# Kernel tuning notes

Hardware: AMD Instinct MI355X
Metric: run time of the kernel (lower is better)

## Reference

```python
import jax, jax.numpy as jnp
import numpy as np

B, IN_DIM, H, E, V, MAX_LEN = 512, 1024, 512, 512, 2048, 32


def setup_inputs() -> dict:
    key = jax.random.key(0)
    ks = jax.random.split(key, 12)
    s = lambda k, shape, scale: (jax.random.normal(k, shape, dtype=jnp.float32) * scale)
    return {
        'x': jax.random.normal(ks[0], (B, IN_DIM), dtype=jnp.float32),
        'agent_w': s(ks[1], (IN_DIM, H), 1.0 / np.sqrt(IN_DIM)),
        'agent_b': jnp.zeros((H,), jnp.float32),
        'sos_embedding': s(ks[2], (E,), 0.01),  # reset_parameters: normal(0, 0.01)
        'embedding': s(ks[3], (V, E), 1.0),
        'w_ih': s(ks[4], (E, 4 * H), 1.0 / np.sqrt(H)),
        'w_hh': s(ks[5], (H, 4 * H), 1.0 / np.sqrt(H)),
        'b_ih': jnp.zeros((4 * H,), jnp.float32),
        'b_hh': jnp.zeros((4 * H,), jnp.float32),
        'out_w': s(ks[6], (H, V), 1.0 / np.sqrt(H)),
        'out_b': jnp.zeros((V,), jnp.float32),
    }


def _unroll(x, agent_w, agent_b, sos_embedding, embedding, w_ih, w_hh, b_ih, b_hh, out_w, out_b):
    h0 = x @ agent_w + agent_b              # agent provides initial hidden [B, H]
    c0 = jnp.zeros_like(h0)
    e0 = jnp.broadcast_to(sos_embedding, (x.shape[0], sos_embedding.shape[0]))
    key0 = jax.random.key(1)

    def step(carry, _):
        h, c, e, key = carry
        key, sk = jax.random.split(key)
        gates = e @ w_ih + h @ w_hh + (b_ih + b_hh)          # [B, 4H], torch gate order i,f,g,o
        i_g, f_g, g_g, o_g = jnp.split(gates, 4, axis=-1)
        c = jax.nn.sigmoid(f_g) * c + jax.nn.sigmoid(i_g) * jnp.tanh(g_g)
        h = jax.nn.sigmoid(o_g) * jnp.tanh(c)
        step_logits = jax.nn.log_softmax(h @ out_w + out_b, axis=-1)  # [B, V]
        probs = jnp.exp(step_logits)
        entropy = -jnp.sum(probs * step_logits, axis=-1)              # Categorical entropy
        sym = jax.random.categorical(sk, step_logits, axis=-1)        # sample [B]
        log_prob = jnp.take_along_axis(step_logits, sym[:, None], axis=1)[:, 0]
        e = embedding[sym]
        return (h, c, e, key), (sym, log_prob, entropy, probs)

    _, (seq, logp, ent, probs) = jax.lax.scan(step, (h0, c0, e0, key0), None, length=MAX_LEN)
    # scan emits leading time dim -> [B, L, ...]
    seq = jnp.transpose(seq, (1, 0))
    logp = jnp.transpose(logp, (1, 0))
    ent = jnp.transpose(ent, (1, 0))
    probs = jnp.transpose(probs, (1, 0, 2))
    # append EOS step (zeros; probs row of ones, as in the source)
    zcol = jnp.zeros((seq.shape[0], 1), jnp.float32)
    seq = jnp.concatenate([seq, zcol.astype(seq.dtype)], axis=1)
    logp = jnp.concatenate([logp, zcol], axis=1)
    ent = jnp.concatenate([ent, zcol], axis=1)
    probs = jnp.concatenate([probs, jnp.ones((probs.shape[0], 1, probs.shape[2]), probs.dtype)], axis=1)
    return seq, probs, logp, ent


def reference(x, agent_w, agent_b, sos_embedding, embedding, w_ih, w_hh, b_ih, b_hh, out_w, out_b):
    return _unroll(x, agent_w, agent_b, sos_embedding, embedding, w_ih, w_hh, b_ih, b_hh, out_w, out_b)
```

## Files before the change

### kernel.cpp

```cpp
#include <hip/hip_runtime.h>
#include <math.h>
#include <stdint.h>
#include <stddef.h>

#define B_ 512
#define H_ 512
#define E_ 512
#define V_ 2048
#define IN_ 1024
#define LSTEPS 32
#define LP1 33

#define TF_PARTITIONABLE 1

#define SPLITK 4
#define SPLITK_H0 16
#define PSTRIDE_GATES (B_ * 2048)
#define PSTRIDE_H0 (B_ * H_)

typedef unsigned short u16;
typedef __attribute__((ext_vector_type(8))) short bhalf8;
typedef __attribute__((ext_vector_type(4))) float f32x4;

__device__ __forceinline__ void tf2x32(uint32_t k0, uint32_t k1,
                                       uint32_t x0, uint32_t x1,
                                       uint32_t& o0, uint32_t& o1) {
  uint32_t ks2 = k0 ^ k1 ^ 0x1BD11BDAu;
  x0 += k0; x1 += k1;
#define TFR(R) { x0 += x1; x1 = (x1 << (R)) | (x1 >> (32 - (R))); x1 ^= x0; }
  TFR(13) TFR(15) TFR(26) TFR(6)
  x0 += k1; x1 += ks2 + 1u;
  TFR(17) TFR(29) TFR(16) TFR(24)
  x0 += ks2; x1 += k0 + 2u;
  TFR(13) TFR(15) TFR(26) TFR(6)
  x0 += k0; x1 += k1 + 3u;
  TFR(17) TFR(29) TFR(16) TFR(24)
  x0 += k1; x1 += ks2 + 4u;
  TFR(13) TFR(15) TFR(26) TFR(6)
  x0 += ks2; x1 += k0 + 5u;
#undef TFR
  o0 = x0; o1 = x1;
}

__global__ void init_keys_kernel(uint32_t* __restrict__ sk) {
  uint32_t k0 = 0u, k1 = 1u;
  for (int t = 0; t < LSTEPS; t++) {
    uint32_t a0, a1, b0, b1;
#if TF_PARTITIONABLE
    tf2x32(k0, k1, 0u, 0u, a0, a1);
    tf2x32(k0, k1, 0u, 1u, b0, b1);
    sk[2 * t] = b0; sk[2 * t + 1] = b1;
    k0 = a0; k1 = a1;
#else
    tf2x32(k0, k1, 0u, 2u, a0, a1);
    tf2x32(k0, k1, 1u, 3u, b0, b1);
    sk[2 * t] = a1; sk[2 * t + 1] = b1;
    k0 = a0; k1 = b0;
#endif
  }
}

__device__ __forceinline__ void split3(float v, u16& h, u16& m, u16& l) {
  uint32_t u = __float_as_uint(v);
  uint32_t r = (u + 0x7FFFu + ((u >> 16) & 1u)) >> 16;
  h = (u16)r;
  float res = v - __uint_as_float(r << 16);
  uint32_t u2 = __float_as_uint(res);
  uint32_t r2 = (u2 + 0x7FFFu + ((u2 >> 16) & 1u)) >> 16;
  m = (u16)r2;
  float res2 = res - __uint_as_float(r2 << 16);
  uint32_t u3 = __float_as_uint(res2);
  uint32_t r3 = (u3 + 0x7FFFu + ((u3 >> 16) & 1u)) >> 16;
  l = (u16)r3;
}

__global__ __launch_bounds__(256) void init_state_planes_kernel(
    const float* __restrict__ sos, float* __restrict__ c,
    u16* __restrict__ eh, u16* __restrict__ em, u16* __restrict__ el) {
  int idx = blockIdx.x * 256 + threadIdx.x;
  if (idx < B_ * H_) {
    c[idx] = 0.0f;
    u16 a, b2, d;
    split3(sos[idx & (E_ - 1)], a, b2, d);
    eh[idx] = a; em[idx] = b2; el[idx] = d;
  }
}

__global__ __launch_bounds__(256) void eos_fill_kernel(
    float* __restrict__ o_seq, float* __restrict__ o_probs,
    float* __restrict__ o_logp, float* __restrict__ o_ent) {
  int b = blockIdx.x, tid = threadIdx.x;
  float* pr = o_probs + ((size_t)b * LP1 + LSTEPS) * V_;
  for (int v = tid; v < V_; v += 256) pr[v] = 1.0f;
  if (tid == 0) {
    o_seq[b * LP1 + LSTEPS] = 0.0f;
    o_logp[b * LP1 + LSTEPS] = 0.0f;
    o_ent[b * LP1 + LSTEPS] = 0.0f;
  }
}

__global__ __launch_bounds__(256) void split_kernel(
    const float* __restrict__ src,
    u16* __restrict__ dh, u16* __restrict__ dm, u16* __restrict__ dl, int n) {
  int i = blockIdx.x * 256 + threadIdx.x;
  if (i < n) {
    u16 a, b2, d;
    split3(src[i], a, b2, d);
    dh[i] = a; dm[i] = b2; dl[i] = d;
  }
}

__global__ __launch_bounds__(256) void transpose_split_kernel(
    const float* __restrict__ src, int srcN,
    u16* __restrict__ dh, u16* __restrict__ dm, u16* __restrict__ dl,
    int dstK, int kOff) {
  __shared__ float t[32][33];
  int tx = threadIdx.x & 31, ty = threadIdx.x >> 5;
  int kt = blockIdx.x * 32, nt = blockIdx.y * 32;
#pragma unroll
  for (int j = 0; j < 4; j++)
    t[ty + j * 8][tx] = src[(size_t)(kt + ty + j * 8) * srcN + nt + tx];
  __syncthreads();
#pragma unroll
  for (int j = 0; j < 4; j++) {
    int n = nt + ty + j * 8;
    int k = kt + tx;
    u16 a, b2, d;
    split3(t[tx][ty + j * 8], a, b2, d);
    size_t o = (size_t)n * dstK + kOff + k;
    dh[o] = a; dm[o] = b2; dl[o] = d;
  }
}

typedef __attribute__((address_space(1))) const void GASV;
typedef __attribute__((address_space(3))) void LASV;
__device__ __forceinline__ void gld16(const void* g, void* l) {
  __builtin_amdgcn_global_load_lds((GASV*)g, (LASV*)l, 16, 0, 0);
}

__global__ __launch_bounds__(256, 1) void gemm3_kernel(
    const u16* __restrict__ A0h, const u16* __restrict__ A0m, const u16* __restrict__ A0l,
    const u16* __restrict__ A1h, const u16* __restrict__ A1m, const u16* __restrict__ A1l,
    int strideA, int kHalf,
    const u16* __restrict__ Bh, const u16* __restrict__ Bm, const u16* __restrict__ Bl,
    int strideB, int N, int KPB,
    float* __restrict__ P, int pstride) {
  __shared__ u16 lds[2][6][4096];
  int tid = threadIdx.x;
  int w = tid >> 6, l = tid & 63;
  int m0 = blockIdx.x * 128, n0 = blockIdx.y * 128;
  int k0 = blockIdx.z * KPB;
  bool hi = (k0 >= kHalf);
  const u16* Ah = hi ? A1h : A0h;
  const u16* Am = hi ? A1m : A0m;
  const u16* Al = hi ? A1l : A0l;
  int kb = hi ? (k0 - kHalf) : k0;

  int srow = l >> 2;
  int slog = (l & 3) ^ ((l >> 3) & 3);
  int seg0 = w * 2, seg1 = w * 2 + 1;
  size_t aG0 = (size_t)(m0 + seg0 * 16 + srow) * strideA + slog * 8;
  size_t aG1 = (size_t)(m0 + seg1 * 16 + srow) * strideA + slog * 8;
  size_t bG0 = (size_t)(n0 + seg0 * 16 + srow) * strideB + slog * 8;
  size_t bG1 = (size_t)(n0 + seg1 * 16 + srow) * strideB + slog * 8;

  int wr = (w >> 1) * 64, wc = (w & 1) * 64;
  int lrow = l & 15, lk8 = l >> 4;
  int xorv = (lrow >> 1) & 3;
  int fOffA = (wr + lrow) * 64 + ((lk8 ^ xorv) << 4);
  int fOffB = (wc + lrow) * 64 + ((lk8 ^ xorv) << 4);

  f32x4 acc[4][4] = {};
  int nch = KPB >> 5;

#define STAGE3(CH, TB) {                                                  \
    int kca = kb + ((CH) << 5);                                           \
    int kcb = k0 + ((CH) << 5);                                           \
    char* Lb = (char*)&lds[TB][0][0];                                     \
    gld16(Ah + aG0 + kca, Lb + 0 * 8192 + seg0 * 1024);                   \
    gld16(Ah + aG1 + kca, Lb + 0 * 8192 + seg1 * 1024);                   \
    gld16(Am + aG0 + kca, Lb + 1 * 8192 + seg0 * 1024);                   \
    gld16(Am + aG1 + kca, Lb + 1 * 8192 + seg1 * 1024);                   \
    gld16(Al + aG0 + kca, Lb + 2 * 8192 + seg0 * 1024);                   \
    gld16(Al + aG1 + kca, Lb + 2 * 8192 + seg1 * 1024);                   \
    gld16(Bh + bG0 + kcb, Lb + 3 * 8192 + seg0 * 1024);                   \
    gld16(Bh + bG1 + kcb, Lb + 3 * 8192 + seg1 * 1024);                   \
    gld16(Bm + bG0 + kcb, Lb + 4 * 8192 + seg0 * 1024);                   \
    gld16(Bm + bG1 + kcb, Lb + 4 * 8192 + seg1 * 1024);                   \
    gld16(Bl + bG0 + kcb, Lb + 5 * 8192 + seg0 * 1024);                   \
    gld16(Bl + bG1 + kcb, Lb + 5 * 8192 + seg1 * 1024);                   \
  }

  STAGE3(0, 0)
  for (int ch = 0; ch < nch; ch++) {
    __syncthreads();
    if (ch + 1 < nch) STAGE3(ch + 1, (ch + 1) & 1)
    const char* base = (const char*)&lds[ch & 1][0][0];
    bhalf8 af[3][4], bfr[3][4];
#pragma unroll
    for (int p = 0; p < 3; p++) {
#pragma unroll
      for (int m = 0; m < 4; m++)
        af[p][m] = *(const bhalf8*)(base + p * 8192 + fOffA + m * 1024);
#pragma unroll
      for (int n = 0; n < 4; n++)
        bfr[p][n] = *(const bhalf8*)(base + (3 + p) * 8192 + fOffB + n * 1024);
    }
    const int PA[6] = {2, 0, 1, 1, 0, 0};
    const int PB[6] = {0, 2, 1, 0, 1, 0};
#pragma unroll
    for (int pp = 0; pp < 6; pp++) {
#pragma unroll
      for (int m = 0; m < 4; m++) {
#pragma unroll
        for (int n = 0; n < 4; n++) {
          acc[m][n] = __builtin_amdgcn_mfma_f32_16x16x32_bf16(
              af[PA[pp]][m], bfr[PB[pp]][n], acc[m][n], 0, 0, 0);
        }
      }
    }
  }
#undef STAGE3

  float* Pb = P + (size_t)blockIdx.z * pstride;
#pragma unroll
  for (int m = 0; m < 4; m++) {
#pragma unroll
    for (int n = 0; n < 4; n++) {
#pragma unroll
      for (int j = 0; j < 4; j++) {
        int row = m0 + wr + m * 16 + lk8 * 4 + j;
        int col = n0 + wc + n * 16 + lrow;
        Pb[(size_t)row * N + col] = acc[m][n][j];
      }
    }
  }
}

__device__ __forceinline__ float sigm(float x) { return 1.0f / (1.0f + expf(-x)); }

__global__ __launch_bounds__(256) void cell_reduce_planes_kernel(
    const float* __restrict__ P,
    const float* __restrict__ b_ih, const float* __restrict__ b_hh,
    float* __restrict__ c,
    u16* __restrict__ hh_, u16* __restrict__ hm_, u16* __restrict__ hl_) {
  int idx = blockIdx.x * 256 + threadIdx.x;
  int b = idx >> 7;
  int h4 = (idx & 127) * 4;
  float4 g4[4];
#pragma unroll
  for (int g = 0; g < 4; g++) {
    size_t off = (size_t)b * 2048 + g * 512 + h4;
    float4 s = *(const float4*)&P[off];
#pragma unroll
    for (int sgl = 1; sgl < SPLITK; sgl++) {
      float4 p = *(const float4*)&P[(size_t)sgl * PSTRIDE_GATES + off];
      s.x += p.x; s.y += p.y; s.z += p.z; s.w += p.w;
    }
    float4 bi = *(const float4*)&b_ih[g * 512 + h4];
    float4 bh = *(const float4*)&b_hh[g * 512 + h4];
    s.x += bi.x + bh.x; s.y += bi.y + bh.y; s.z += bi.z + bh.z; s.w += bi.w + bh.w;
    g4[g] = s;
  }
  size_t ci = (size_t)b * 512 + h4;
  float4 cold = *(const float4*)&c[ci];
  float4 cn;
  float hv[4];
  {
    const float* ig = (const float*)&g4[0];
    const float* fg = (const float*)&g4[1];
    const float* gg = (const float*)&g4[2];
    const float* og = (const float*)&g4[3];
    float* cc = (float*)&cn;
    const float* co = (const float*)&cold;
#pragma unroll
    for (int k = 0; k < 4; k++) {
      float cv = sigm(fg[k]) * co[k] + sigm(ig[k]) * tanhf(gg[k]);
      cc[k] = cv;
      hv[k] = sigm(og[k]) * tanhf(cv);
    }
  }
  *(float4*)&c[ci] = cn;
  ushort4 vh, vm, vl;
  u16 a, b2, d;
  split3(hv[0], a, b2, d); vh.x = a; vm.x = b2; vl.x = d;
  split3(hv[1], a, b2, d); vh.y = a; vm.y = b2; vl.y = d;
  split3(hv[2], a, b2, d); vh.z = a; vm.z = b2; vl.z = d;
  split3(hv[3], a, b2, d); vh.w = a; vm.w = b2; vl.w = d;
  *(ushort4*)&hh_[ci] = vh;
  *(ushort4*)&hm_[ci] = vm;
  *(ushort4*)&hl_[ci] = vl;
}

__global__ __launch_bounds__(256) void reduce_bias_planes_kernel(
    const float* __restrict__ P, int pstride, int nsplit,
    const float* __restrict__ bias,
    u16* __restrict__ oh, u16* __restrict__ om, u16* __restrict__ ol) {
  int idx = blockIdx.x * 256 + threadIdx.x;
  if (idx >= B_ * H_ / 4) return;
  size_t off = (size_t)idx * 4;
  float4 s = *(const float4*)&P[off];
  for (int sgl = 1; sgl < nsplit; sgl++) {
    float4 p = *(const float4*)&P[(size_t)sgl * pstride + off];
    s.x += p.x; s.y += p.y; s.z += p.z; s.w += p.w;
  }
  int col = (int)(off & (H_ - 1));
  float4 bv = *(const float4*)&bias[col];
  s.x += bv.x; s.y += bv.y; s.z += bv.z; s.w += bv.w;
  ushort4 vh, vm, vl;
  u16 a, b2, d;
  split3(s.x, a, b2, d); vh.x = a; vm.x = b2; vl.x = d;
  split3(s.y, a, b2, d); vh.y = a; vm.y = b2; vl.y = d;
  split3(s.z, a, b2, d); vh.z = a; vm.z = b2; vl.z = d;
  split3(s.w, a, b2, d); vh.w = a; vm.w = b2; vl.w = d;
  *(ushort4*)&oh[off] = vh;
  *(ushort4*)&om[off] = vm;
  *(ushort4*)&ol[off] = vl;
}

__global__ __launch_bounds__(256) void sample_step_kernel(
    const float* __restrict__ P, const float* __restrict__ out_b,
    const uint32_t* __restrict__ skv,
    const u16* __restrict__ ebH, const u16* __restrict__ ebM, const u16* __restrict__ ebL,
    u16* __restrict__ eh, u16* __restrict__ em_, u16* __restrict__ el_,
    float* __restrict__ o_seq, float* __restrict__ o_probs,
    float* __restrict__ o_logp, float* __restrict__ o_ent, int t) {
  __shared__ float zs[V_];
  __shared__ float rmax[4], rsum[4], rps[4], rav[4];
  __shared__ int rai[4];
  int tid = threadIdx.x, b = blockIdx.x;
  int wid = tid >> 6;
  const float* pr0 = P + (size_t)b * V_ + tid * 8;
  float4 za = *(const float4*)pr0;
  float4 zb = *(const float4*)(pr0 + 4);
#pragma unroll
  for (int s = 1; s < SPLITK; s++) {
    float4 pa = *(const float4*)(pr0 + (size_t)s * PSTRIDE_GATES);
    float4 pb = *(const float4*)(pr0 + (size_t)s * PSTRIDE_GATES + 4);
    za.x += pa.x; za.y += pa.y; za.z += pa.z; za.w += pa.w;
    zb.x += pb.x; zb.y += pb.y; zb.z += pb.z; zb.w += pb.w;
  }
  {
    float4 oa = *(const float4*)(out_b + tid * 8);
    float4 ob = *(const float4*)(out_b + tid * 8 + 4);
    za.x += oa.x; za.y += oa.y; za.z += oa.z; za.w += oa.w;
    zb.x += ob.x; zb.y += ob.y; zb.z += ob.z; zb.w += ob.w;
  }
  float zv[8] = {za.x, za.y, za.z, za.w, zb.x, zb.y, zb.z, zb.w};
  *(float4*)&zs[tid * 8] = za;
  *(float4*)&zs[tid * 8 + 4] = zb;

  float m = zv[0];
#pragma unroll
  for (int i = 1; i < 8; i++) m = fmaxf(m, zv[i]);
  for (int off = 32; off; off >>= 1) m = fmaxf(m, __shfl_xor(m, off));
  if ((tid & 63) == 0) rmax[wid] = m;
  __syncthreads();
  m = fmaxf(fmaxf(rmax[0], rmax[1]), fmaxf(rmax[2], rmax[3]));

  float sh[8];
  float ssum = 0.f;
#pragma unroll
  for (int i = 0; i < 8; i++) { sh[i] = zv[i] - m; ssum += expf(sh[i]); }
  for (int off = 32; off; off >>= 1) ssum += __shfl_xor(ssum, off);
  if ((tid & 63) == 0) rsum[wid] = ssum;
  __syncthreads();
  float S = (rsum[0] + rsum[1]) + (rsum[2] + rsum[3]);
  float ls = logf(S);

  uint32_t sk0 = skv[2 * t], sk1 = skv[2 * t + 1];
  float psum = 0.f;
  float best = -INFINITY;
  int bi = 0;
  float pv[8];
#pragma unroll
  for (int i = 0; i < 8; i++) {
    float s = sh[i] - ls;
    float p = expf(s);
    pv[i] = p;
    psum += p * s;
    int v = tid * 8 + i;
    uint32_t o0, o1, bits;
#if TF_PARTITIONABLE
    uint32_t j = (uint32_t)(b * V_ + v);
    tf2x32(sk0, sk1, 0u, j, o0, o1);
    bits = o0 ^ o1;
#else
    uint32_t j = (uint32_t)(b * V_ + v);
    const uint32_t n2 = (uint32_t)(B_ * V_ / 2);
    if (j < n2) { tf2x32(sk0, sk1, j, j + n2, o0, o1); bits = o0; }
    else       { tf2x32(sk0, sk1, j - n2, j, o0, o1); bits = o1; }
#endif
    float f = __uint_as_float((bits >> 9) | 0x3f800000u) - 1.0f;
    float u = fmaxf(f, 1.17549435e-38f);
    float g = -logf(-logf(u));
    float a = s + g;
    if (a > best) { best = a; bi = v; }
  }
  float* prw = o_probs + ((size_t)b * LP1 + t) * V_ + tid * 8;
  *(float4*)prw = make_float4(pv[0], pv[1], pv[2], pv[3]);
  *(float4*)(prw + 4) = make_float4(pv[4], pv[5], pv[6], pv[7]);

  for (int off = 32; off; off >>= 1) psum += __shfl_xor(psum, off);
  for (int off = 32; off; off >>= 1) {
    float ov = __shfl_xor(best, off);
    int oi = __shfl_xor(bi, off);
    if (ov > best || (ov == best && oi < bi)) { best = ov; bi = oi; }
  }
  if ((tid & 63) == 0) { rps[wid] = psum; rav[wid] = best; rai[wid] = bi; }
  __syncthreads();
  float ent = -((rps[0] + rps[1]) + (rps[2] + rps[3]));
  float bv2 = rav[0]; int sym = rai[0];
#pragma unroll
  for (int w2 = 1; w2 < 4; w2++) {
    if (rav[w2] > bv2 || (rav[w2] == bv2 && rai[w2] < sym)) { bv2 = rav[w2]; sym = rai[w2]; }
  }
  const u16* gh = ebH + (size_t)sym * E_;
  const u16* gm = ebM + (size_t)sym * E_;
  const u16* gl = ebL + (size_t)sym * E_;
  for (int k2 = tid; k2 < E_; k2 += 256) {
    eh[(size_t)b * E_ + k2]  = gh[k2];
    em_[(size_t)b * E_ + k2] = gm[k2];
    el_[(size_t)b * E_ + k2] = gl[k2];
  }
  if (tid == 0) {
    float s_sym = (zs[sym] - m) - ls;
    o_seq[b * LP1 + t] = (float)sym;
    o_logp[b * LP1 + t] = s_sym;
    o_ent[b * LP1 + t] = ent;
  }
}

extern "C" void kernel_launch(void* const* d_in, const int* in_sizes, int n_in,
                              void* d_out, int out_size, void* d_ws, size_t ws_size,
                              hipStream_t stream) {
  (void)in_sizes; (void)n_in; (void)out_size; (void)ws_size;
  const float* x     = (const float*)d_in[0];
  const float* agw   = (const float*)d_in[1];
  const float* agb   = (const float*)d_in[2];
  const float* sos   = (const float*)d_in[3];
  const float* emb   = (const float*)d_in[4];
  const float* w_ih  = (const float*)d_in[5];
  const float* w_hh  = (const float*)d_in[6];
  const float* b_ih  = (const float*)d_in[7];
  const float* b_hh  = (const float*)d_in[8];
  const float* out_w = (const float*)d_in[9];
  const float* out_b = (const float*)d_in[10];

  char* w = (char*)d_ws;
  size_t o = 0;
  uint32_t* sk = (uint32_t*)(w + o); o += 1024;
  float* c = (float*)(w + o);        o += (size_t)B_ * H_ * 4;
#define PLANE3(name, elems) \
  u16* name##H = (u16*)(w + o); o += (size_t)(elems) * 2; \
  u16* name##M = (u16*)(w + o); o += (size_t)(elems) * 2; \
  u16* name##L = (u16*)(w + o); o += (size_t)(elems) * 2;
  PLANE3(e,  B_ * E_)
  PLANE3(hA, B_ * H_)
  PLANE3(hB, B_ * H_)
  PLANE3(xp, B_ * IN_)
  PLANE3(aw, H_ * IN_)
  PLANE3(gw, 2048 * IN_)
  PLANE3(ow, V_ * H_)
  PLANE3(eb, V_ * E_)
#undef PLANE3
  float* P = (float*)(w + o);

  float* out = (float*)d_out;
  float* o_seq   = out;
  float* o_probs = out + (size_t)B_ * LP1;
  float* o_logp  = o_probs + (size_t)B_ * LP1 * V_;
  float* o_ent   = o_logp + (size_t)B_ * LP1;

  const int BIG = 1 << 30;

  init_keys_kernel<<<1, 1, 0, stream>>>(sk);
  init_state_planes_kernel<<<(B_ * H_ + 255) / 256, 256, 0, stream>>>(sos, c, eH, eM, eL);
  eos_fill_kernel<<<B_, 256, 0, stream>>>(o_seq, o_probs, o_logp, o_ent);

  split_kernel<<<(B_ * IN_ + 255) / 256, 256, 0, stream>>>(x, xpH, xpM, xpL, B_ * IN_);
  split_kernel<<<(V_ * E_ + 255) / 256, 256, 0, stream>>>(emb, ebH, ebM, ebL, V_ * E_);
  transpose_split_kernel<<<dim3(512 / 32, 2048 / 32), 256, 0, stream>>>(
      w_ih, 2048, gwH, gwM, gwL, 1024, 0);
  transpose_split_kernel<<<dim3(512 / 32, 2048 / 32), 256, 0, stream>>>(
      w_hh, 2048, gwH, gwM, gwL, 1024, 512);
  transpose_split_kernel<<<dim3(512 / 32, 2048 / 32), 256, 0, stream>>>(
      out_w, 2048, owH, owM, owL, 512, 0);
  transpose_split_kernel<<<dim3(1024 / 32, 512 / 32), 256, 0, stream>>>(
      agw, 512, awH, awM, awL, 1024, 0);

  gemm3_kernel<<<dim3(4, 4, SPLITK_H0), 256, 0, stream>>>(
      xpH, xpM, xpL, xpH, xpM, xpL, IN_, BIG,
      awH, awM, awL, IN_, H_, IN_ / SPLITK_H0, P, PSTRIDE_H0);
  reduce_bias_planes_kernel<<<(B_ * H_ / 4 + 255) / 256, 256, 0, stream>>>(
      P, PSTRIDE_H0, SPLITK_H0, agb, hAH, hAM, hAL);

  for (int t = 0; t < LSTEPS; t++) {
    u16 *hiH = (t & 1) ? hBH : hAH, *hiM = (t & 1) ? hBM : hAM, *hiL = (t & 1) ? hBL : hAL;
    u16 *hoH = (t & 1) ? hAH : hBH, *hoM = (t & 1) ? hAM : hBM, *hoL = (t & 1) ? hAL : hBL;
    gemm3_kernel<<<dim3(4, 16, SPLITK), 256, 0, stream>>>(
        eH, eM, eL, hiH, hiM, hiL, E_, E_,
        gwH, gwM, gwL, IN_, 2048, (E_ + H_) / SPLITK, P, PSTRIDE_GATES);
    cell_reduce_planes_kernel<<<B_ * H_ / 4 / 256, 256, 0, stream>>>(
        P, b_ih, b_hh, c, hoH, hoM, hoL);
    gemm3_kernel<<<dim3(4, 16, SPLITK), 256, 0, stream>>>(
        hoH, hoM, hoL, hoH, hoM, hoL, H_, BIG,
        owH, owM, owL, H_, 2048, H_ / SPLITK, P, PSTRIDE_GATES);
    sample_step_kernel<<<B_, 256, 0, stream>>>(
        P, out_b, sk, ebH, ebM, ebL, eH, eM, eL,
        o_seq, o_probs, o_logp, o_ent, t);
  }
}
```

Baseline: 1.723 ms.

## Replace split-K 128x128 GEMM with full-K 64x64 tiles and XCD-aware block mapping

The three-plane bf16 GEMM moves from 128x128 tiles with split-K partial sums to 64x64 tiles that each run the full K loop and write the final result directly. This removes the partial-sum buffers and the extra reduction reads in the cell and sampling kernels. Block indices are remapped so that blocks sharing an N column land on the same XCD, which is meant to improve L2 reuse of weight tiles. The trade-off is smaller tiles with less operand reuse per block and longer serial K loops, in exchange for fewer memory passes and higher occupancy.

```diff
diff --git a/kernel.cpp b/kernel.cpp
--- a/kernel.cpp
+++ b/kernel.cpp
@@ -12,11 +12,6 @@
 #define LP1 33
 
 #define TF_PARTITIONABLE 1
-
-#define SPLITK 4
-#define SPLITK_H0 16
-#define PSTRIDE_GATES (B_ * 2048)
-#define PSTRIDE_H0 (B_ * H_)
 
 typedef unsigned short u16;
 typedef __attribute__((ext_vector_type(8))) short bhalf8;
@@ -138,100 +133,92 @@
   __builtin_amdgcn_global_load_lds((GASV*)g, (LASV*)l, 16, 0, 0);
 }
 
-__global__ __launch_bounds__(256, 1) void gemm3_kernel(
+__global__ __launch_bounds__(256, 3) void gemm64_kernel(
     const u16* __restrict__ A0h, const u16* __restrict__ A0m, const u16* __restrict__ A0l,
     const u16* __restrict__ A1h, const u16* __restrict__ A1m, const u16* __restrict__ A1l,
     int strideA, int kHalf,
     const u16* __restrict__ Bh, const u16* __restrict__ Bm, const u16* __restrict__ Bl,
-    int strideB, int N, int KPB,
-    float* __restrict__ P, int pstride) {
-  __shared__ u16 lds[2][6][4096];
+    int strideB, int N, int K, int gridN,
+    float* __restrict__ C) {
+  __shared__ __align__(16) char lds[2][24576];
   int tid = threadIdx.x;
   int w = tid >> 6, l = tid & 63;
-  int m0 = blockIdx.x * 128, n0 = blockIdx.y * 128;
-  int k0 = blockIdx.z * KPB;
-  bool hi = (k0 >= kHalf);
-  const u16* Ah = hi ? A1h : A0h;
-  const u16* Am = hi ? A1m : A0m;
-  const u16* Al = hi ? A1l : A0l;
-  int kb = hi ? (k0 - kHalf) : k0;
+  int bid = blockIdx.x;
+  int xcd = bid & 7, mIdx = (bid >> 3) & 7, cIdx = bid >> 6;
+  int nIdx = xcd * (gridN >> 3) + cIdx;
+  int m0 = mIdx * 64, n0 = nIdx * 64;
 
   int srow = l >> 2;
   int slog = (l & 3) ^ ((l >> 3) & 3);
-  int seg0 = w * 2, seg1 = w * 2 + 1;
-  size_t aG0 = (size_t)(m0 + seg0 * 16 + srow) * strideA + slog * 8;
-  size_t aG1 = (size_t)(m0 + seg1 * 16 + srow) * strideA + slog * 8;
-  size_t bG0 = (size_t)(n0 + seg0 * 16 + srow) * strideB + slog * 8;
-  size_t bG1 = (size_t)(n0 + seg1 * 16 + srow) * strideB + slog * 8;
-
-  int wr = (w >> 1) * 64, wc = (w & 1) * 64;
+  size_t aRow = (size_t)(m0 + w * 16 + srow) * strideA + slog * 8;
+  size_t bRow = (size_t)(n0 + w * 16 + srow) * strideB + slog * 8;
+
   int lrow = l & 15, lk8 = l >> 4;
   int xorv = (lrow >> 1) & 3;
+  int wr = (w >> 1) * 32, wc = (w & 1) * 32;
   int fOffA = (wr + lrow) * 64 + ((lk8 ^ xorv) << 4);
   int fOffB = (wc + lrow) * 64 + ((lk8 ^ xorv) << 4);
 
-  f32x4 acc[4][4] = {};
-  int nch = KPB >> 5;
-
-#define STAGE3(CH, TB) {                                                  \
-    int kca = kb + ((CH) << 5);                                           \
-    int kcb = k0 + ((CH) << 5);                                           \
-    char* Lb = (char*)&lds[TB][0][0];                                     \
-    gld16(Ah + aG0 + kca, Lb + 0 * 8192 + seg0 * 1024);                   \
-    gld16(Ah + aG1 + kca, Lb + 0 * 8192 + seg1 * 1024);                   \
-    gld16(Am + aG0 + kca, Lb + 1 * 8192 + seg0 * 1024);                   \
-    gld16(Am + aG1 + kca, Lb + 1 * 8192 + seg1 * 1024);                   \
-    gld16(Al + aG0 + kca, Lb + 2 * 8192 + seg0 * 1024);                   \
-    gld16(Al + aG1 + kca, Lb + 2 * 8192 + seg1 * 1024);                   \
-    gld16(Bh + bG0 + kcb, Lb + 3 * 8192 + seg0 * 1024);                   \
-    gld16(Bh + bG1 + kcb, Lb + 3 * 8192 + seg1 * 1024);                   \
-    gld16(Bm + bG0 + kcb, Lb + 4 * 8192 + seg0 * 1024);                   \
-    gld16(Bm + bG1 + kcb, Lb + 4 * 8192 + seg1 * 1024);                   \
-    gld16(Bl + bG0 + kcb, Lb + 5 * 8192 + seg0 * 1024);                   \
-    gld16(Bl + bG1 + kcb, Lb + 5 * 8192 + seg1 * 1024);                   \
-  }
-
-  STAGE3(0, 0)
+  f32x4 acc[2][2] = {};
+  int nch = K >> 5;
+
+#define STAGE64(CH, TB) {                                               \
+    int kc = (CH) << 5;                                                 \
+    bool hi2 = kc >= kHalf;                                             \
+    const u16* Ah2 = hi2 ? A1h : A0h;                                   \
+    const u16* Am2 = hi2 ? A1m : A0m;                                   \
+    const u16* Al2 = hi2 ? A1l : A0l;                                   \
+    size_t ao = aRow + (hi2 ? kc - kHalf : kc);                         \
+    size_t bo = bRow + kc;                                              \
+    char* Lb = (char*)&lds[TB][0] + w * 1024;                           \
+    gld16(Ah2 + ao, Lb + 0 * 4096);                                     \
+    gld16(Am2 + ao, Lb + 1 * 4096);                                     \
+    gld16(Al2 + ao, Lb + 2 * 4096);                                     \
+    gld16(Bh + bo, Lb + 3 * 4096);                                      \
+    gld16(Bm + bo, Lb + 4 * 4096);                                      \
+    gld16(Bl + bo, Lb + 5 * 4096);                                      \
+  }
+
+  STAGE64(0, 0)
   for (int ch = 0; ch < nch; ch++) {
     __syncthreads();
-    if (ch + 1 < nch) STAGE3(ch + 1, (ch + 1) & 1)
-    const char* base = (const char*)&lds[ch & 1][0][0];
-    bhalf8 af[3][4], bfr[3][4];
+    if (ch + 1 < nch) STAGE64(ch + 1, (ch + 1) & 1)
+    const char* base = (const char*)&lds[ch & 1][0];
+    bhalf8 af[3][2], bfr[3][2];
 #pragma unroll
     for (int p = 0; p < 3; p++) {
 #pragma unroll
-      for (int m = 0; m < 4; m++)
-        af[p][m] = *(const bhalf8*)(base + p * 8192 + fOffA + m * 1024);
-#pragma unroll
-      for (int n = 0; n < 4; n++)
-        bfr[p][n] = *(const bhalf8*)(base + (3 + p) * 8192 + fOffB + n * 1024);
+      for (int m = 0; m < 2; m++)
+        af[p][m] = *(const bhalf8*)(base + p * 4096 + fOffA + m * 1024);
+#pragma unroll
+      for (int n = 0; n < 2; n++)
+        bfr[p][n] = *(const bhalf8*)(base + (3 + p) * 4096 + fOffB + n * 1024);
     }
     const int PA[6] = {2, 0, 1, 1, 0, 0};
     const int PB[6] = {0, 2, 1, 0, 1, 0};
 #pragma unroll
     for (int pp = 0; pp < 6; pp++) {
 #pragma unroll
-      for (int m = 0; m < 4; m++) {
-#pragma unroll
-        for (int n = 0; n < 4; n++) {
+      for (int m = 0; m < 2; m++) {
+#pragma unroll
+        for (int n = 0; n < 2; n++) {
           acc[m][n] = __builtin_amdgcn_mfma_f32_16x16x32_bf16(
               af[PA[pp]][m], bfr[PB[pp]][n], acc[m][n], 0, 0, 0);
         }
       }
     }
   }
-#undef STAGE3
-
-  float* Pb = P + (size_t)blockIdx.z * pstride;
-#pragma unroll
-  for (int m = 0; m < 4; m++) {
-#pragma unroll
-    for (int n = 0; n < 4; n++) {
+#undef STAGE64
+
+#pragma unroll
+  for (int m = 0; m < 2; m++) {
+#pragma unroll
+    for (int n = 0; n < 2; n++) {
 #pragma unroll
       for (int j = 0; j < 4; j++) {
         int row = m0 + wr + m * 16 + lk8 * 4 + j;
         int col = n0 + wc + n * 16 + lrow;
-        Pb[(size_t)row * N + col] = acc[m][n][j];
+        C[(size_t)row * N + col] = acc[m][n][j];
       }
     }
   }
@@ -240,7 +227,7 @@
 __device__ __forceinline__ float sigm(float x) { return 1.0f / (1.0f + expf(-x)); }
 
 __global__ __launch_bounds__(256) void cell_reduce_planes_kernel(
-    const float* __restrict__ P,
+    const float* __restrict__ G,
     const float* __restrict__ b_ih, const float* __restrict__ b_hh,
     float* __restrict__ c,
     u16* __restrict__ hh_, u16* __restrict__ hm_, u16* __restrict__ hl_) {
@@ -251,12 +238,7 @@
 #pragma unroll
   for (int g = 0; g < 4; g++) {
     size_t off = (size_t)b * 2048 + g * 512 + h4;
-    float4 s = *(const float4*)&P[off];
-#pragma unroll
-    for (int sgl = 1; sgl < SPLITK; sgl++) {
-      float4 p = *(const float4*)&P[(size_t)sgl * PSTRIDE_GATES + off];
-      s.x += p.x; s.y += p.y; s.z += p.z; s.w += p.w;
-    }
+    float4 s = *(const float4*)&G[off];
     float4 bi = *(const float4*)&b_ih[g * 512 + h4];
     float4 bh = *(const float4*)&b_hh[g * 512 + h4];
     s.x += bi.x + bh.x; s.y += bi.y + bh.y; s.z += bi.z + bh.z; s.w += bi.w + bh.w;
@@ -319,7 +301,7 @@
 }
 
 __global__ __launch_bounds__(256) void sample_step_kernel(
-    const float* __restrict__ P, const float* __restrict__ out_b,
+    const float* __restrict__ Z, const float* __restrict__ out_b,
     const uint32_t* __restrict__ skv,
     const u16* __restrict__ ebH, const u16* __restrict__ ebM, const u16* __restrict__ ebL,
     u16* __restrict__ eh, u16* __restrict__ em_, u16* __restrict__ el_,
@@ -330,16 +312,9 @@
   __shared__ int rai[4];
   int tid = threadIdx.x, b = blockIdx.x;
   int wid = tid >> 6;
-  const float* pr0 = P + (size_t)b * V_ + tid * 8;
+  const float* pr0 = Z + (size_t)b * V_ + tid * 8;
   float4 za = *(const float4*)pr0;
   float4 zb = *(const float4*)(pr0 + 4);
-#pragma unroll
-  for (int s = 1; s < SPLITK; s++) {
-    float4 pa = *(const float4*)(pr0 + (size_t)s * PSTRIDE_GATES);
-    float4 pb = *(const float4*)(pr0 + (size_t)s * PSTRIDE_GATES + 4);
-    za.x += pa.x; za.y += pa.y; za.z += pa.z; za.w += pa.w;
-    zb.x += pb.x; zb.y += pb.y; zb.z += pb.z; zb.w += pb.w;
-  }
   {
     float4 oa = *(const float4*)(out_b + tid * 8);
     float4 ob = *(const float4*)(out_b + tid * 8 + 4);
@@ -489,23 +464,23 @@
   transpose_split_kernel<<<dim3(1024 / 32, 512 / 32), 256, 0, stream>>>(
       agw, 512, awH, awM, awL, 1024, 0);
 
-  gemm3_kernel<<<dim3(4, 4, SPLITK_H0), 256, 0, stream>>>(
+  gemm64_kernel<<<64, 256, 0, stream>>>(
       xpH, xpM, xpL, xpH, xpM, xpL, IN_, BIG,
-      awH, awM, awL, IN_, H_, IN_ / SPLITK_H0, P, PSTRIDE_H0);
+      awH, awM, awL, IN_, H_, IN_, 8, P);
   reduce_bias_planes_kernel<<<(B_ * H_ / 4 + 255) / 256, 256, 0, stream>>>(
-      P, PSTRIDE_H0, SPLITK_H0, agb, hAH, hAM, hAL);
+      P, 0, 1, agb, hAH, hAM, hAL);
 
   for (int t = 0; t < LSTEPS; t++) {
     u16 *hiH = (t & 1) ? hBH : hAH, *hiM = (t & 1) ? hBM : hAM, *hiL = (t & 1) ? hBL : hAL;
     u16 *hoH = (t & 1) ? hAH : hBH, *hoM = (t & 1) ? hAM : hBM, *hoL = (t & 1) ? hAL : hBL;
-    gemm3_kernel<<<dim3(4, 16, SPLITK), 256, 0, stream>>>(
+    gemm64_kernel<<<256, 256, 0, stream>>>(
         eH, eM, eL, hiH, hiM, hiL, E_, E_,
-        gwH, gwM, gwL, IN_, 2048, (E_ + H_) / SPLITK, P, PSTRIDE_GATES);
+        gwH, gwM, gwL, IN_, 2048, IN_, 32, P);
     cell_reduce_planes_kernel<<<B_ * H_ / 4 / 256, 256, 0, stream>>>(
         P, b_ih, b_hh, c, hoH, hoM, hoL);
-    gemm3_kernel<<<dim3(4, 16, SPLITK), 256, 0, stream>>>(
+    gemm64_kernel<<<256, 256, 0, stream>>>(
         hoH, hoM, hoL, hoH, hoM, hoL, H_, BIG,
-        owH, owM, owL, H_, 2048, H_ / SPLITK, P, PSTRIDE_GATES);
+        owH, owM, owL, H_, 2048, H_, 32, P);
     sample_step_kernel<<<B_, 256, 0, stream>>>(
         P, out_b, sk, ebH, ebM, ebL, eH, eM, eL,
         o_seq, o_probs, o_logp, o_ent, t);
```

After: 1.737 ms. Within noise of the previous version (+0.8%).
